# Performance work log

Hardware: AMD Instinct MI355X
Metric: run time of the kernel (lower is better)

## Reference

```python
import jax, jax.numpy as jnp
import numpy as np

SEQ, D_IN, D_KQ, D_V = 4096, 1024, 1024, 1024

def setup_inputs() -> dict:
    key = jax.random.key(0)
    k1, k2, k3, k4 = jax.random.split(key, 4)
    return {
        "x": jax.random.normal(k1, (SEQ, D_IN), dtype=jnp.float32),
        "W_query": jax.random.uniform(k2, (D_IN, D_KQ), dtype=jnp.float32),
        "W_key": jax.random.uniform(k3, (D_IN, D_KQ), dtype=jnp.float32),
        "W_value": jax.random.uniform(k4, (D_IN, D_V), dtype=jnp.float32),
    }

def reference(x, W_query, W_key, W_value):
    d_out_kq = W_query.shape[1]
    Q = x @ W_query          # [S, d_kq]
    K = x @ W_key            # [S, d_kq]
    V = x @ W_value          # [S, d_v]
    attn = Q @ K.T           # [S, S]
    S = attn.shape[0]
    causal_mask = jnp.triu(jnp.ones((S, S), dtype=bool), k=1)
    masked = jnp.where(causal_mask, -jnp.inf, attn)
    attn_weights = jax.nn.softmax(masked / jnp.sqrt(jnp.float32(d_out_kq)), axis=1)
    return attn_weights @ V  # [S, d_v]
```

## Files before the change

### kernel.cpp

```cpp
#include <hip/hip_runtime.h>
#include <math.h>

#define SQ 4096
#define DD 1024
#define TRI 528

typedef _Float16 f16;
typedef f16 f16x8 __attribute__((ext_vector_type(8)));
typedef f16 f16x4 __attribute__((ext_vector_type(4)));
typedef float f32x4 __attribute__((ext_vector_type(4)));

__device__ __forceinline__ float waveMax(float v) {
#pragma unroll
    for (int o = 32; o > 0; o >>= 1) v = fmaxf(v, __shfl_down(v, o, 64));
    return v;
}
__device__ __forceinline__ float waveSum(float v) {
#pragma unroll
    for (int o = 32; o > 0; o >>= 1) v += __shfl_down(v, o, 64);
    return v;
}

__device__ __forceinline__ void gl_lds16(const f16* g, f16* l) {
    __builtin_amdgcn_global_load_lds(
        (const __attribute__((address_space(1))) void*)g,
        (__attribute__((address_space(3))) void*)l, 16, 0, 0);
}

template<int NRW>
__device__ __forceinline__ void stage(const f16* src, int ldk, f16* lds, int w, int lane) {
    const int r0 = w * NRW + (lane >> 2);
    const f16* g = src + (size_t)r0 * ldk + ((lane & 3) << 3);
    f16* l = lds + w * NRW * 32;
    gl_lds16(g, l);
    if (NRW == 32) gl_lds16(g + (size_t)ldk * 16, l + 16 * 32);
}

template<int MODE>
__global__ __launch_bounds__(256)
void gemm_k(const f16* __restrict__ Ah, const f16* __restrict__ Al,
            const f16* __restrict__ Bh, const f16* __restrict__ Bl,
            float* __restrict__ Cf,
            f16* __restrict__ Qh, f16* __restrict__ Ql,
            f16* __restrict__ Kh, f16* __restrict__ Kl,
            f16* __restrict__ Vt, float scale)
{
    constexpr int TM = (MODE == 2) ? 64 : 128;
    constexpr int NI = (MODE == 2) ? 2 : 4;
    constexpr int H  = (MODE == 2) ? 2 : 1;
    constexpr int AH = TM * 32;
    constexpr int BH = 128 * 32;
    constexpr int SMSZ = (MODE == 2) ? H * (AH + BH) : 2 * H * (AH + BH);

    int bm, bn, tri = 0, half = 0;
    if (MODE == 1) {
        const int id = blockIdx.x;
        half = id & 1;
        tri = id >> 1;
        bm = (int)((sqrtf(8.f * (float)tri + 1.f) - 1.f) * 0.5f);
        while ((bm + 1) * (bm + 2) / 2 <= tri) ++bm;
        while (bm * (bm + 1) / 2 > tri) --bm;
        bn = tri - bm * (bm + 1) / 2;
    } else if (MODE == 2) {
        bn = blockIdx.x;
        bm = (int)gridDim.y - 1 - (int)blockIdx.y;
    } else {
        bn = blockIdx.x; bm = blockIdx.y;
    }

    const int m0 = bm * TM;
    const int n0 = bn << 7;
    const int lda = (MODE == 2) ? 128 : DD;
    const int ldb = (MODE == 2) ? SQ : DD;
    const int kst = (MODE == 1) ? (half << 9) : 0;
    const int kend = (MODE == 1) ? (kst + 512)
                   : (MODE == 2) ? (((bm >> 1) + 1) << 7) : DD;
    const bool dolo = (MODE == 1) || (MODE == 0 && bn < 16);

    __shared__ f16 sm[SMSZ];
    f16* smA  = sm;
    f16* smB  = sm + H * AH;
    f16* smAl = sm + H * (AH + BH);
    f16* smBl = smAl + H * AH;

    const int tid = threadIdx.x;
    const int w = tid >> 6, lane = tid & 63;
    const int wr = (MODE == 2) ? 0 : ((w >> 1) << 6);
    const int wc = (MODE == 2) ? (w << 5) : ((w & 1) << 6);
    const int fcol = lane & 15, quad = lane >> 4;

    f32x4 acc[4][NI];
#pragma unroll
    for (int i = 0; i < 4; ++i)
#pragma unroll
        for (int j = 0; j < NI; ++j) acc[i][j] = (f32x4){0.f, 0.f, 0.f, 0.f};

    const int bmT = (MODE == 2) ? (bm >> 1) : 0;
    const size_t triRow = (MODE == 2) ? (size_t)(bmT * (bmT + 1) / 2) : 0;
    const f16* Ab  = Ah + (size_t)m0 * ((MODE == 2) ? 0 : DD);
    const f16* Bb  = Bh + (size_t)n0 * ldb;
    const f16* Abl = dolo ? Al + (size_t)m0 * DD : nullptr;
    const f16* Bbl = dolo ? Bl + (size_t)n0 * ldb : nullptr;

    for (int k0 = kst; k0 < kend; k0 += 32 * H) {
        __syncthreads();
#pragma unroll
        for (int h = 0; h < H; ++h) {
            const int kk = k0 + 32 * h;
            const f16* as;
            if (MODE == 2) {
                as = Ah + ((triRow + (size_t)(kk >> 7)) << 14)
                        + ((size_t)(m0 & 127) << 7) + (kk & 127);
            } else {
                as = Ab + kk;
            }
            stage<TM / 4>(as, lda, smA + h * AH, w, lane);
            stage<32>(Bb + kk, ldb, smB + h * BH, w, lane);
            if (dolo) {
                stage<TM / 4>(Abl + kk, DD, smAl + h * AH, w, lane);
                stage<32>(Bbl + kk, ldb, smBl + h * BH, w, lane);
            }
        }
        __syncthreads();

#pragma unroll
        for (int h = 0; h < H; ++h) {
            f16x8 bh[NI], bl[NI];
#pragma unroll
            for (int in = 0; in < NI; ++in) {
                const int off = ((wc + (in << 4) + fcol) << 5) + (quad << 3);
                bh[in] = *(const f16x8*)&smB[h * BH + off];
                if (dolo) bl[in] = *(const f16x8*)&smBl[h * BH + off];
            }
#pragma unroll
            for (int im = 0; im < 4; ++im) {
                const int off = ((wr + (im << 4) + fcol) << 5) + (quad << 3);
                f16x8 ah = *(const f16x8*)&smA[h * AH + off];
                f16x8 al;
                if (dolo) al = *(const f16x8*)&smAl[h * AH + off];
#pragma unroll
                for (int in = 0; in < NI; ++in) {
                    if (dolo) {
                        acc[im][in] = __builtin_amdgcn_mfma_f32_16x16x32_f16(ah, bl[in], acc[im][in], 0, 0, 0);
                        acc[im][in] = __builtin_amdgcn_mfma_f32_16x16x32_f16(al, bh[in], acc[im][in], 0, 0, 0);
                    }
                    acc[im][in] = __builtin_amdgcn_mfma_f32_16x16x32_f16(ah, bh[in], acc[im][in], 0, 0, 0);
                }
            }
        }
    }

#pragma unroll
    for (int im = 0; im < 4; ++im) {
#pragma unroll
        for (int in = 0; in < NI; ++in) {
            if (MODE == 0) {
                const int region = bn >> 3;
                const int colL = ((bn & 7) << 7) + wc + (in << 4) + fcol;
                if (region == 2) {
                    const int tc = m0 + wr + (im << 4) + (quad << 2);
                    f16x4 o;
#pragma unroll
                    for (int r = 0; r < 4; ++r) o[r] = (f16)acc[im][in][r];
                    *(f16x4*)&Vt[(size_t)colL * SQ + tc] = o;
                } else {
                    f16* Hh = region ? Kh : Qh;
                    f16* Hl = region ? Kl : Ql;
#pragma unroll
                    for (int r = 0; r < 4; ++r) {
                        const int row = m0 + wr + (im << 4) + (quad << 2) + r;
                        const float v = acc[im][in][r];
                        const f16 h = (f16)v;
                        Hh[(size_t)row * DD + colL] = h;
                        Hl[(size_t)row * DD + colL] = (f16)(v - (float)h);
                    }
                }
            } else if (MODE == 1) {
                float* Cp = Cf + (((size_t)half * TRI + tri) << 14);
#pragma unroll
                for (int r = 0; r < 4; ++r) {
                    const int rl = wr + (im << 4) + (quad << 2) + r;
                    const int cl = wc + (in << 4) + fcol;
                    Cp[(rl << 7) + cl] = acc[im][in][r] * scale;
                }
            } else {
#pragma unroll
                for (int r = 0; r < 4; ++r) {
                    const int row = m0 + wr + (im << 4) + (quad << 2) + r;
                    const int col = n0 + wc + (in << 4) + fcol;
                    Cf[(size_t)row * DD + col] = acc[im][in][r];
                }
            }
        }
    }
}

__global__ __launch_bounds__(256)
void split_f32(const float* __restrict__ x, f16* __restrict__ h, f16* __restrict__ l, int n)
{
    const int i = (blockIdx.x * 256 + threadIdx.x) * 4;
    if (i >= n) return;
    const float4 v = *(const float4*)(x + i);
    const f16 h0 = (f16)v.x, h1 = (f16)v.y, h2 = (f16)v.z, h3 = (f16)v.w;
    f16x4 hv = {h0, h1, h2, h3};
    f16x4 lv = {(f16)(v.x - (float)h0), (f16)(v.y - (float)h1),
                (f16)(v.z - (float)h2), (f16)(v.w - (float)h3)};
    *(f16x4*)(h + i) = hv;
    *(f16x4*)(l + i) = lv;
}

__global__ __launch_bounds__(256)
void transpose_split3(const float* __restrict__ W0, const float* __restrict__ W1,
                      const float* __restrict__ W2,
                      f16* __restrict__ Th0, f16* __restrict__ Tl0,
                      int K, int N)
{
    const float* W = (blockIdx.z == 0) ? W0 : (blockIdx.z == 1) ? W1 : W2;
    f16* Th = Th0 + (size_t)blockIdx.z * K * N;
    f16* Tl = Tl0 + (size_t)blockIdx.z * K * N;

    __shared__ float t[64][65];
    const int n0 = blockIdx.x << 6, k0 = blockIdx.y << 6;
    const int tx = threadIdx.x & 63, ty = threadIdx.x >> 6;
    for (int r = ty; r < 64; r += 4) t[r][tx] = W[(size_t)(k0 + r) * N + n0 + tx];
    __syncthreads();
    for (int r = ty; r < 64; r += 4) {
        const float v = t[tx][r];
        const f16 h = (f16)v;
        Th[(size_t)(n0 + r) * K + k0 + tx] = h;
        Tl[(size_t)(n0 + r) * K + k0 + tx] = (f16)(v - (float)h);
    }
}

__global__ __launch_bounds__(256)
void softmax_causal(const float* __restrict__ A0, f16* __restrict__ P)
{
    const int i = blockIdx.x;
    const int n = i + 1;
    const int tid = threadIdx.x, w = tid >> 6, lane = tid & 63;
    __shared__ float redM[4], redS[4];
    __shared__ float rowbuf[SQ];

    const int bmI = i >> 7;
    const size_t base = ((size_t)(bmI * (bmI + 1) / 2) << 14) + ((size_t)(i & 127) << 7);
    const float* A1 = A0 + ((size_t)TRI << 14);

    float m = -INFINITY;
    for (int j = tid; j < n; j += 256) {
        const size_t a = base + ((size_t)(j >> 7) << 14) + (j & 127);
        const float v = A0[a] + A1[a];
        rowbuf[j] = v;
        m = fmaxf(m, v);
    }
    m = waveMax(m);
    if (lane == 0) redM[w] = m;
    __syncthreads();
    const float mAll = fmaxf(fmaxf(redM[0], redM[1]), fmaxf(redM[2], redM[3]));

    float s = 0.f;
    for (int j = tid; j < n; j += 256) {
        const float e = __expf(rowbuf[j] - mAll);
        rowbuf[j] = e;
        s += e;
    }
    s = waveSum(s);
    if (lane == 0) redS[w] = s;
    __syncthreads();
    const float inv = 1.0f / (redS[0] + redS[1] + redS[2] + redS[3]);

    const int kmax = (bmI + 1) << 7;
    for (int j = tid; j < kmax; j += 256) {
        const size_t a = base + ((size_t)(j >> 7) << 14) + (j & 127);
        P[a] = (j < n) ? (f16)(rowbuf[j] * inv) : (f16)0.f;
    }
}

extern "C" void kernel_launch(void* const* d_in, const int* in_sizes, int n_in,
                              void* d_out, int out_size, void* d_ws, size_t ws_size,
                              hipStream_t stream)
{
    const float* x  = (const float*)d_in[0];
    const float* Wq = (const float*)d_in[1];
    const float* Wk = (const float*)d_in[2];
    const float* Wv = (const float*)d_in[3];
    float* out = (float*)d_out;

    char* p = (char*)d_ws;
    auto take = [&](size_t bytes) { void* r = (void*)p; p += (bytes + 255) & ~(size_t)255; return r; };
    const size_t SD = (size_t)SQ * DD;
    f16* xh  = (f16*)take(SD * 2);
    f16* xl  = (f16*)take(SD * 2);
    f16* Wth = (f16*)take((size_t)3 * DD * DD * 2);
    f16* Wtl = (f16*)take((size_t)3 * DD * DD * 2);
    f16* Qh  = (f16*)take(SD * 2);
    f16* Ql  = (f16*)take(SD * 2);
    f16* Kh  = (f16*)take(SD * 2);
    f16* Kl  = (f16*)take(SD * 2);
    f16* Vt  = (f16*)take(SD * 2);
    float* attn = (float*)take((size_t)2 * TRI * 16384 * 4);
    f16* P   = (f16*)take((size_t)TRI * 16384 * 2);

    const dim3 blk(256);

    split_f32<<<dim3(SD / 4 / 256), blk, 0, stream>>>(x, xh, xl, (int)SD);
    transpose_split3<<<dim3(DD / 64, DD / 64, 3), blk, 0, stream>>>(
        Wq, Wk, Wv, Wth, Wtl, DD, DD);

    gemm_k<0><<<dim3(24, SQ / 128), blk, 0, stream>>>(
        xh, xl, Wth, Wtl, nullptr, Qh, Ql, Kh, Kl, Vt, 1.0f);

    gemm_k<1><<<dim3(2 * TRI), blk, 0, stream>>>(
        Qh, Ql, Kh, Kl, attn, nullptr, nullptr, nullptr, nullptr, nullptr, 0.03125f);

    softmax_causal<<<dim3(SQ), blk, 0, stream>>>(attn, P);

    gemm_k<2><<<dim3(DD / 128, SQ / 64), blk, 0, stream>>>(
        P, nullptr, Vt, nullptr, out, nullptr, nullptr, nullptr, nullptr, nullptr, 1.0f);
}
```

Baseline: 300.4 us.

## Fuse prepass kernels, remap GEMM block order, vectorize causal softmax

Merges the x split and weight transpose-split into one launch to save a kernel launch. Remaps block indices for the QK^T GEMM, interleaving tiles across groups of eight so neighbouring blocks spread over different tiles, and swaps grid axes in the PV GEMM so consecutive blocks walk row tiles. Vectorizes the softmax loads, exp and stores to float4 and half4. The block remap and the vector accesses depend on alignment and on how blocks get dispatched to XCDs.

Result: no change. 301.4 us (+0.3%).

```diff
diff --git a/kernel.cpp b/kernel.cpp
--- a/kernel.cpp
+++ b/kernel.cpp
@@ -54,16 +54,16 @@
 
     int bm, bn, tri = 0, half = 0;
     if (MODE == 1) {
-        const int id = blockIdx.x;
-        half = id & 1;
-        tri = id >> 1;
+        const int lin = ((int)blockIdx.x & 7) * 132 + ((int)blockIdx.x >> 3);
+        half = lin & 1;
+        tri = lin >> 1;
         bm = (int)((sqrtf(8.f * (float)tri + 1.f) - 1.f) * 0.5f);
         while ((bm + 1) * (bm + 2) / 2 <= tri) ++bm;
         while (bm * (bm + 1) / 2 > tri) --bm;
         bn = tri - bm * (bm + 1) / 2;
     } else if (MODE == 2) {
-        bn = blockIdx.x;
-        bm = (int)gridDim.y - 1 - (int)blockIdx.y;
+        bm = 63 - (int)blockIdx.x;
+        bn = blockIdx.y;
     } else {
         bn = blockIdx.x; bm = blockIdx.y;
     }
@@ -196,39 +196,42 @@
 }
 
 __global__ __launch_bounds__(256)
-void split_f32(const float* __restrict__ x, f16* __restrict__ h, f16* __restrict__ l, int n)
+void prepass(const float* __restrict__ x,
+             const float* __restrict__ W0, const float* __restrict__ W1,
+             const float* __restrict__ W2,
+             f16* __restrict__ xh, f16* __restrict__ xl,
+             f16* __restrict__ Th0, f16* __restrict__ Tl0)
 {
-    const int i = (blockIdx.x * 256 + threadIdx.x) * 4;
-    if (i >= n) return;
-    const float4 v = *(const float4*)(x + i);
-    const f16 h0 = (f16)v.x, h1 = (f16)v.y, h2 = (f16)v.z, h3 = (f16)v.w;
-    f16x4 hv = {h0, h1, h2, h3};
-    f16x4 lv = {(f16)(v.x - (float)h0), (f16)(v.y - (float)h1),
-                (f16)(v.z - (float)h2), (f16)(v.w - (float)h3)};
-    *(f16x4*)(h + i) = hv;
-    *(f16x4*)(l + i) = lv;
-}
-
-__global__ __launch_bounds__(256)
-void transpose_split3(const float* __restrict__ W0, const float* __restrict__ W1,
-                      const float* __restrict__ W2,
-                      f16* __restrict__ Th0, f16* __restrict__ Tl0,
-                      int K, int N)
-{
-    const float* W = (blockIdx.z == 0) ? W0 : (blockIdx.z == 1) ? W1 : W2;
-    f16* Th = Th0 + (size_t)blockIdx.z * K * N;
-    f16* Tl = Tl0 + (size_t)blockIdx.z * K * N;
-
     __shared__ float t[64][65];
-    const int n0 = blockIdx.x << 6, k0 = blockIdx.y << 6;
-    const int tx = threadIdx.x & 63, ty = threadIdx.x >> 6;
-    for (int r = ty; r < 64; r += 4) t[r][tx] = W[(size_t)(k0 + r) * N + n0 + tx];
+    const int id = blockIdx.x;
+    const int tid = threadIdx.x;
+
+    if (id < 4096) {
+        const int i = (id * 256 + tid) * 4;
+        const float4 v = *(const float4*)(x + i);
+        const f16 h0 = (f16)v.x, h1 = (f16)v.y, h2 = (f16)v.z, h3 = (f16)v.w;
+        f16x4 hv = {h0, h1, h2, h3};
+        f16x4 lv = {(f16)(v.x - (float)h0), (f16)(v.y - (float)h1),
+                    (f16)(v.z - (float)h2), (f16)(v.w - (float)h3)};
+        *(f16x4*)(xh + i) = hv;
+        *(f16x4*)(xl + i) = lv;
+        return;
+    }
+
+    const int tt = id - 4096;
+    const int z = tt >> 8, r8 = tt & 255;
+    const float* W = (z == 0) ? W0 : (z == 1) ? W1 : W2;
+    f16* Th = Th0 + (size_t)z * DD * DD;
+    f16* Tl = Tl0 + (size_t)z * DD * DD;
+    const int n0 = (r8 & 15) << 6, k0 = (r8 >> 4) << 6;
+    const int tx = tid & 63, ty = tid >> 6;
+    for (int r = ty; r < 64; r += 4) t[r][tx] = W[(size_t)(k0 + r) * DD + n0 + tx];
     __syncthreads();
     for (int r = ty; r < 64; r += 4) {
         const float v = t[tx][r];
         const f16 h = (f16)v;
-        Th[(size_t)(n0 + r) * K + k0 + tx] = h;
-        Tl[(size_t)(n0 + r) * K + k0 + tx] = (f16)(v - (float)h);
+        Th[(size_t)(n0 + r) * DD + k0 + tx] = h;
+        Tl[(size_t)(n0 + r) * DD + k0 + tx] = (f16)(v - (float)h);
     }
 }
 
@@ -245,8 +248,18 @@
     const size_t base = ((size_t)(bmI * (bmI + 1) / 2) << 14) + ((size_t)(i & 127) << 7);
     const float* A1 = A0 + ((size_t)TRI << 14);
 
+    const int nv = n >> 2;
     float m = -INFINITY;
-    for (int j = tid; j < n; j += 256) {
+    for (int g = tid; g < nv; g += 256) {
+        const int j = g << 2;
+        const size_t a = base + ((size_t)(j >> 7) << 14) + (j & 127);
+        const float4 v0 = *(const float4*)(A0 + a);
+        const float4 v1 = *(const float4*)(A1 + a);
+        float4 v = make_float4(v0.x + v1.x, v0.y + v1.y, v0.z + v1.z, v0.w + v1.w);
+        *(f32x4*)&rowbuf[j] = (f32x4){v.x, v.y, v.z, v.w};
+        m = fmaxf(m, fmaxf(fmaxf(v.x, v.y), fmaxf(v.z, v.w)));
+    }
+    for (int j = (nv << 2) + tid; j < n; j += 256) {
         const size_t a = base + ((size_t)(j >> 7) << 14) + (j & 127);
         const float v = A0[a] + A1[a];
         rowbuf[j] = v;
@@ -258,7 +271,15 @@
     const float mAll = fmaxf(fmaxf(redM[0], redM[1]), fmaxf(redM[2], redM[3]));
 
     float s = 0.f;
-    for (int j = tid; j < n; j += 256) {
+    for (int g = tid; g < nv; g += 256) {
+        const int j = g << 2;
+        f32x4 v = *(f32x4*)&rowbuf[j];
+        v[0] = __expf(v[0] - mAll); v[1] = __expf(v[1] - mAll);
+        v[2] = __expf(v[2] - mAll); v[3] = __expf(v[3] - mAll);
+        *(f32x4*)&rowbuf[j] = v;
+        s += v[0] + v[1] + v[2] + v[3];
+    }
+    for (int j = (nv << 2) + tid; j < n; j += 256) {
         const float e = __expf(rowbuf[j] - mAll);
         rowbuf[j] = e;
         s += e;
@@ -269,7 +290,15 @@
     const float inv = 1.0f / (redS[0] + redS[1] + redS[2] + redS[3]);
 
     const int kmax = (bmI + 1) << 7;
-    for (int j = tid; j < kmax; j += 256) {
+    for (int g = tid; g < nv; g += 256) {
+        const int j = g << 2;
+        const size_t a = base + ((size_t)(j >> 7) << 14) + (j & 127);
+        const f32x4 v = *(const f32x4*)&rowbuf[j];
+        f16x4 o = {(f16)(v[0] * inv), (f16)(v[1] * inv),
+                   (f16)(v[2] * inv), (f16)(v[3] * inv)};
+        *(f16x4*)&P[a] = o;
+    }
+    for (int j = (nv << 2) + tid; j < kmax; j += 256) {
         const size_t a = base + ((size_t)(j >> 7) << 14) + (j & 127);
         P[a] = (j < n) ? (f16)(rowbuf[j] * inv) : (f16)0.f;
     }
@@ -302,9 +331,7 @@
 
     const dim3 blk(256);
 
-    split_f32<<<dim3(SD / 4 / 256), blk, 0, stream>>>(x, xh, xl, (int)SD);
-    transpose_split3<<<dim3(DD / 64, DD / 64, 3), blk, 0, stream>>>(
-        Wq, Wk, Wv, Wth, Wtl, DD, DD);
+    prepass<<<dim3(4096 + 768), blk, 0, stream>>>(x, Wq, Wk, Wv, xh, xl, Wth, Wtl);
 
     gemm_k<0><<<dim3(24, SQ / 128), blk, 0, stream>>>(
         xh, xl, Wth, Wtl, nullptr, Qh, Ql, Kh, Kl, Vt, 1.0f);
@@ -314,6 +341,6 @@
 
     softmax_causal<<<dim3(SQ), blk, 0, stream>>>(attn, P);
 
-    gemm_k<2><<<dim3(DD / 128, SQ / 64), blk, 0, stream>>>(
+    gemm_k<2><<<dim3(SQ / 64, DD / 128), blk, 0, stream>>>(
         P, nullptr, Vt, nullptr, out, nullptr, nullptr, nullptr, nullptr, nullptr, 1.0f);
 }
```
